# Optimization experiments

Measured on AMD Instinct MI355X. Metric: run time of the kernel, lower is better.

The kernel has to match this reference:

```python
import jax, jax.numpy as jnp
import numpy as np

# tcnn Hash-grid config from TropicalHashGrid.__init__ defaults
L = 16          # n_levels
F = 2           # n_features_per_level
T = 19          # log2_hashmap_size
N_MIN = 16      # base_resolution
N_MAX = 2048
SCALE = 1.0
HASHMAP = 1 << T
B = 2.0 ** (np.log2(N_MAX * SCALE / N_MIN) / (L - 1))  # per-level scale
PRIMES = np.array([1, 2654435761, 805459861], dtype=np.uint32)
# 8 trilinear corner offsets in {0,1}^3
CORNERS = np.stack(np.meshgrid(*([np.arange(2)] * 3), indexing='ij'), axis=-1).reshape(8, 3)
N_POINTS = 2 ** 21


def _level_encode(x, tbl, scale, res, dense):
    """One hash-grid level: x [N,3], tbl [HASHMAP,F] -> [N,F]."""
    pos = x * scale + 0.5                      # tcnn convention
    pf = jnp.floor(pos)
    frac = pos - pf                            # [N,3]
    grid = pf.astype(jnp.int32)                # [N,3]
    idx = grid[:, None, :] + jnp.asarray(CORNERS, jnp.int32)[None]  # [N,8,3]
    if dense:
        # coarse level fits densely: stride indexing x + y*res + z*res^2
        idx = jnp.minimum(idx, res - 1)
        flat = idx[..., 0] + idx[..., 1] * res + idx[..., 2] * (res * res)
    else:
        # spatial hash: xor of coordinate * prime, masked to table size
        u = idx.astype(jnp.uint32)
        flat = ((u[..., 0] * PRIMES[0]) ^ (u[..., 1] * PRIMES[1]) ^ (u[..., 2] * PRIMES[2]))
        flat = (flat & jnp.uint32(HASHMAP - 1)).astype(jnp.int32)
    feats = tbl[flat]                          # [N,8,F] gather
    c = jnp.asarray(CORNERS, jnp.float32)
    w = jnp.prod(jnp.where(c[None] > 0, frac[:, None, :], 1.0 - frac[:, None, :]), axis=-1)  # [N,8]
    return jnp.einsum('nc,ncf->nf', w, feats)  # trilinear blend


def setup_inputs() -> dict:
    key = jax.random.key(0)
    k1, k2 = jax.random.split(key)
    x = jax.random.uniform(k1, (N_POINTS, 3), dtype=jnp.float32)  # coords in [0,1)^3
    # hash table params (tcnn inits ~U(-1e-4,1e-4); scaled randn equivalent scale)
    table = jax.random.normal(k2, (L, HASHMAP, F), dtype=jnp.float32) * 1e-4
    return {"x": x, "table": table}


def reference(x, table):
    outs = []
    for l in range(L):
        scale = float(N_MIN * (B ** l) - 1.0)   # grid_scale per tcnn/_marks
        res = int(np.ceil(scale)) + 1
        dense = (res ** 3) <= HASHMAP
        outs.append(_level_encode(x, table[l], scale, res, dense))
    return jnp.concatenate(outs, axis=-1)        # [N, L*F]
```

## Files before the change

### kernel.cpp

```cpp
#include <hip/hip_runtime.h>
#include <cstdint>
#include <cmath>


typedef float    f32x2 __attribute__((ext_vector_type(2)));
typedef float    f32x4 __attribute__((ext_vector_type(4)));
typedef uint32_t u32x2 __attribute__((ext_vector_type(2)));
typedef uint32_t u32x4 __attribute__((ext_vector_type(4)));
typedef _Float16 h16x2 __attribute__((ext_vector_type(2)));

#define NLEVELS 16
#define HASHMAP (1 << 19)
#define HMASK ((uint32_t)(HASHMAP - 1))
#define PRIME_Y 2654435761u
#define PRIME_Z 805459861u
#define F16SCALE 1024.0f
#define F16UNSCALE (1.0f / 1024.0f)

struct HGParams {
    float scale[NLEVELS];
    int   res[NLEVELS];
    int   dense[NLEVELS];
    int   dpk_off[NLEVELS];
    int   hq_off[NLEVELS];
    int   dq_off[NLEVELS];
};

__device__ __forceinline__ uint32_t sel4(u32x4 q, uint32_t k) {
    const uint32_t a = (k & 1u) ? q.y : q.x;
    const uint32_t b = (k & 1u) ? q.w : q.z;
    return (k & 2u) ? b : a;
}
__device__ __forceinline__ void unpack_h2(uint32_t w, float& lo, float& hi) {
    const h16x2 h = __builtin_bit_cast(h16x2, w);
    lo = (float)h.x; hi = (float)h.y;
}
__device__ __forceinline__ uint32_t pack_h2(float a, float b) {
    h16x2 h; h.x = (_Float16)a; h.y = (_Float16)b;
    return __builtin_bit_cast(uint32_t, h);
}

__global__ __launch_bounds__(256) void repack_hashed_f16(
    const f32x4* __restrict__ table2, uint32_t* __restrict__ hqw, HGParams p)
{
    const int l = blockIdx.y;
    if (p.hq_off[l] < 0) return;
    const f32x4* __restrict__ src = table2 + (size_t)l * (HASHMAP / 2);
    u32x2* __restrict__ dst = (u32x2*)(hqw + (size_t)p.hq_off[l] * 4);
    for (int k = blockIdx.x * 256 + threadIdx.x; k < HASHMAP / 2;
         k += gridDim.x * 256) {
        const f32x4 v = src[k];
        u32x2 w;
        w.x = pack_h2(v.x * F16SCALE, v.y * F16SCALE);
        w.y = pack_h2(v.z * F16SCALE, v.w * F16SCALE);
        dst[k] = w;
    }
}

__global__ __launch_bounds__(256) void repack_dense_f16(
    const f32x2* __restrict__ table, u32x4* __restrict__ dqt, HGParams p)
{
    const int l = blockIdx.y;
    if (p.dq_off[l] < 0) return;
    const int res = p.res[l];
    const int rm = res - 1;
    const int r2 = res * res;
    const int res3 = r2 * res;
    const f32x2* __restrict__ src = table + (size_t)l * HASHMAP;
    u32x4* __restrict__ dst = dqt + p.dq_off[l];
    for (int k = blockIdx.x * 256 + threadIdx.x; k < res3;
         k += gridDim.x * 256) {
        const int x = k % res;
        const int t = k / res;
        const int y = t % res;
        const int dx = (x < rm) ? 1 : 0;
        const int dy = (y < rm) ? res : 0;
        const f32x2 e00 = src[k];
        const f32x2 e10 = src[k + dx];
        const f32x2 e01 = src[k + dy];
        const f32x2 e11 = src[k + dx + dy];
        u32x4 w;
        w.x = pack_h2(e00.x * F16SCALE, e00.y * F16SCALE);
        w.y = pack_h2(e10.x * F16SCALE, e10.y * F16SCALE);
        w.z = pack_h2(e01.x * F16SCALE, e01.y * F16SCALE);
        w.w = pack_h2(e11.x * F16SCALE, e11.y * F16SCALE);
        dst[k] = w;
    }
}

__global__ __launch_bounds__(256) void repack_dense_k(
    const f32x2* __restrict__ table, f32x4* __restrict__ dpk, HGParams p)
{
    const int l = blockIdx.y;
    if (!p.dense[l] || p.dpk_off[l] < 0) return;
    const int res = p.res[l];
    const int res3 = res * res * res;
    const f32x2* __restrict__ src = table + (size_t)l * HASHMAP;
    f32x4* __restrict__ dst = dpk + p.dpk_off[l];
    for (int k = blockIdx.x * 256 + threadIdx.x; k < res3; k += gridDim.x * 256) {
        const f32x2 a = src[k];
        const f32x2 b = src[k + 1];
        f32x4 v; v.x = a.x; v.y = a.y; v.z = b.x; v.w = b.y;
        dst[k] = v;
    }
}

__device__ __forceinline__ void point_fp32(
    const f32x2* __restrict__ tbl, const f32x4* __restrict__ dpkt,
    bool dense, int res,
    float rx, float ry, float rz, int ix, int iy, int iz,
    float& ox, float& oy)
{
    const float wx0 = 1.0f - rx, wx1 = rx;
    const float wy_[2] = {1.0f - ry, ry};
    const float wz_[2] = {1.0f - rz, rz};
    float ax = 0.0f, ay = 0.0f;
    if (dense) {
        const int rm = res - 1;
        const int x0 = min(ix, rm), x1 = min(ix + 1, rm);
        const int y0 = min(iy, rm), y1 = min(iy + 1, rm);
        const int z0 = min(iz, rm), z1 = min(iz + 1, rm);
        const int r2 = res * res;
        const int ys[2] = {y0 * res, y1 * res};
        const int zs[2] = {z0 * r2,  z1 * r2};
        const int d = x1 - x0;
        if (dpkt) {
            f32x4 f4[4];
#pragma unroll
            for (int c = 0; c < 4; ++c)
                f4[c] = dpkt[x0 + ys[(c >> 1) & 1] + zs[c & 1]];
#pragma unroll
            for (int c = 0; c < 4; ++c) {
                const f32x2 c0 = f4[c].xy;
                const f32x2 c1 = d ? f4[c].zw : f4[c].xy;
                const float wyz = wy_[(c >> 1) & 1] * wz_[c & 1];
                ax += wyz * (wx0 * c0.x + wx1 * c1.x);
                ay += wyz * (wx0 * c0.y + wx1 * c1.y);
            }
        } else {
            f32x2 f0[4], f1[4];
#pragma unroll
            for (int c = 0; c < 4; ++c) {
                const int b = ys[(c >> 1) & 1] + zs[c & 1];
                f0[c] = tbl[x0 + b];
                f1[c] = tbl[x1 + b];
            }
#pragma unroll
            for (int c = 0; c < 4; ++c) {
                const float wyz = wy_[(c >> 1) & 1] * wz_[c & 1];
                ax += wyz * (wx0 * f0[c].x + wx1 * f1[c].x);
                ay += wyz * (wx0 * f0[c].y + wx1 * f1[c].y);
            }
        }
    } else {
        const uint32_t ux = (uint32_t)ix;
        const uint32_t hy[2] = {(uint32_t)iy * PRIME_Y, (uint32_t)(iy + 1) * PRIME_Y};
        const uint32_t hz[2] = {(uint32_t)iz * PRIME_Z, (uint32_t)(iz + 1) * PRIME_Z};
        uint32_t H0[4], H1[4];
#pragma unroll
        for (int c = 0; c < 4; ++c) {
            const uint32_t hyz = hy[(c >> 1) & 1] ^ hz[c & 1];
            H0[c] = (ux ^ hyz) & HMASK;
            H1[c] = ((ux + 1u) ^ hyz) & HMASK;
        }
        const f32x4* __restrict__ t4 = (const f32x4*)tbl;
        f32x4 f4[4];
#pragma unroll
        for (int c = 0; c < 4; ++c) f4[c] = t4[H0[c] >> 1];
        f32x2 c1v[4];
        if (ux & 1u) {
#pragma unroll
            for (int c = 0; c < 4; ++c) c1v[c] = tbl[H1[c]];
        } else {
#pragma unroll
            for (int c = 0; c < 4; ++c)
                c1v[c] = (H0[c] & 1u) ? f4[c].xy : f4[c].zw;
        }
#pragma unroll
        for (int c = 0; c < 4; ++c) {
            const f32x2 c0 = (H0[c] & 1u) ? f4[c].zw : f4[c].xy;
            const float wyz = wy_[(c >> 1) & 1] * wz_[c & 1];
            ax += wyz * (wx0 * c0.x + wx1 * c1v[c].x);
            ay += wyz * (wx0 * c0.y + wx1 * c1v[c].y);
        }
    }
    ox = ax; oy = ay;
}

__global__ __launch_bounds__(256, 6) void hashgrid_level(
    const float* __restrict__ x,
    const float* __restrict__ table,
    const f32x4* __restrict__ dpk,
    const u32x4* __restrict__ hq,
    const u32x4* __restrict__ dq,
    f32x2* __restrict__ dst,
    HGParams p,
    int npoints,
    size_t stride_l,
    size_t stride_n)
{
    __shared__ float sx[1536];
    const int tid = threadIdx.x;
    const int base = blockIdx.x << 9;
    const int l = blockIdx.y;

    const int total = npoints * 3;
    const int sbase = base * 3;
#pragma unroll
    for (int k = 0; k < 6; ++k) {
        const int li = tid + (k << 8);
        const int gi = sbase + li;
        sx[li] = (gi < total) ? x[gi] : 0.0f;
    }
    __syncthreads();

    const int n0 = base + (tid << 1);
    if (n0 >= npoints) return;
    const bool pair = (n0 + 1) < npoints;

    const float scale = p.scale[l];
    const int   res   = p.res[l];
    const bool  dense = (p.dense[l] != 0);

    float rx[2], ry[2], rz[2];
    int ixv[2], iyv[2], izv[2];
#pragma unroll
    for (int j = 0; j < 2; ++j) {
        const int s = ((tid << 1) | j) * 3;
        const float px = sx[s + 0] * scale + 0.5f;
        const float py = sx[s + 1] * scale + 0.5f;
        const float pz = sx[s + 2] * scale + 0.5f;
        const float fx = floorf(px), fy = floorf(py), fz = floorf(pz);
        rx[j] = px - fx; ry[j] = py - fy; rz[j] = pz - fz;
        ixv[j] = (int)fx; iyv[j] = (int)fy; izv[j] = (int)fz;
    }

    float ox[2], oy[2];

    if (dense && dq && p.dq_off[l] >= 0) {
        const u32x4* __restrict__ dt = dq + p.dq_off[l];
        const int rm = res - 1, r2 = res * res;
        u32x4 qa[2], qb[2];
#pragma unroll
        for (int j = 0; j < 2; ++j) {
            const int x0 = min(ixv[j], rm), y0 = min(iyv[j], rm);
            const int z0 = min(izv[j], rm), z1 = min(izv[j] + 1, rm);
            const int b = x0 + y0 * res;
            qa[j] = dt[b + z0 * r2];
            qb[j] = dt[b + z1 * r2];
        }
#pragma unroll
        for (int j = 0; j < 2; ++j) {
            const float wx0 = 1.0f - rx[j], wx1 = rx[j];
            const float wy0 = 1.0f - ry[j], wy1 = ry[j];
            const float wz0 = 1.0f - rz[j], wz1 = rz[j];
            float a00x, a00y, a10x, a10y, a01x, a01y, a11x, a11y;
            unpack_h2(qa[j].x, a00x, a00y);
            unpack_h2(qa[j].y, a10x, a10y);
            unpack_h2(qa[j].z, a01x, a01y);
            unpack_h2(qa[j].w, a11x, a11y);
            const float bax = wy0 * (wx0 * a00x + wx1 * a10x)
                            + wy1 * (wx0 * a01x + wx1 * a11x);
            const float bay = wy0 * (wx0 * a00y + wx1 * a10y)
                            + wy1 * (wx0 * a01y + wx1 * a11y);
            float b00x, b00y, b10x, b10y, b01x, b01y, b11x, b11y;
            unpack_h2(qb[j].x, b00x, b00y);
            unpack_h2(qb[j].y, b10x, b10y);
            unpack_h2(qb[j].z, b01x, b01y);
            unpack_h2(qb[j].w, b11x, b11y);
            const float bbx = wy0 * (wx0 * b00x + wx1 * b10x)
                            + wy1 * (wx0 * b01x + wx1 * b11x);
            const float bby = wy0 * (wx0 * b00y + wx1 * b10y)
                            + wy1 * (wx0 * b01y + wx1 * b11y);
            ox[j] = (wz0 * bax + wz1 * bbx) * F16UNSCALE;
            oy[j] = (wz0 * bay + wz1 * bby) * F16UNSCALE;
        }
    } else if (!dense && hq && p.hq_off[l] >= 0) {
        const u32x4* __restrict__ ht = hq + p.hq_off[l];
        const uint32_t* __restrict__ htw = (const uint32_t*)ht;
        uint32_t H0[2][4], dxm[2];
#pragma unroll
        for (int j = 0; j < 2; ++j) {
            const uint32_t ux = (uint32_t)ixv[j];
            const uint32_t hy0 = (uint32_t)iyv[j] * PRIME_Y;
            const uint32_t hy1 = (uint32_t)(iyv[j] + 1) * PRIME_Y;
            const uint32_t hz0 = (uint32_t)izv[j] * PRIME_Z;
            const uint32_t hz1 = (uint32_t)(izv[j] + 1) * PRIME_Z;
#pragma unroll
            for (int c = 0; c < 4; ++c) {
                const uint32_t hyz = ((c & 2) ? hy1 : hy0) ^ ((c & 1) ? hz1 : hz0);
                H0[j][c] = (ux ^ hyz) & HMASK;
            }
            dxm[j] = (ux ^ (ux + 1u)) & HMASK;
        }
        u32x4 q0[2][4];
#pragma unroll
        for (int j = 0; j < 2; ++j)
#pragma unroll
            for (int c = 0; c < 4; ++c)
                q0[j][c] = ht[H0[j][c] >> 2];
        uint32_t sE[2][4];
#pragma unroll
        for (int j = 0; j < 2; ++j) {
            if (dxm[j] >= 4u) {
#pragma unroll
                for (int c = 0; c < 4; ++c)
                    sE[j][c] = htw[H0[j][c] ^ dxm[j]];
            }
        }
#pragma unroll
        for (int j = 0; j < 2; ++j) {
            const float wx0 = 1.0f - rx[j], wx1 = rx[j];
            const float wy0 = 1.0f - ry[j], wy1 = ry[j];
            const float wz0 = 1.0f - rz[j], wz1 = rz[j];
            const bool st = (dxm[j] >= 4u);
            float ax = 0.0f, ay = 0.0f;
#pragma unroll
            for (int c = 0; c < 4; ++c) {
                const uint32_t k0 = H0[j][c] & 3u;
                const uint32_t e0 = sel4(q0[j][c], k0);
                const uint32_t e1 = st ? sE[j][c]
                                       : sel4(q0[j][c], k0 ^ (dxm[j] & 3u));
                float c0x, c0y, c1x, c1y;
                unpack_h2(e0, c0x, c0y);
                unpack_h2(e1, c1x, c1y);
                const float wyz = ((c & 2) ? wy1 : wy0) * ((c & 1) ? wz1 : wz0);
                ax += wyz * (wx0 * c0x + wx1 * c1x);
                ay += wyz * (wx0 * c0y + wx1 * c1y);
            }
            ox[j] = ax * F16UNSCALE;
            oy[j] = ay * F16UNSCALE;
        }
    } else {
        const f32x2* __restrict__ tbl =
            (const f32x2*)table + (size_t)l * (size_t)HASHMAP;
        const f32x4* __restrict__ dpkt =
            (dense && dpk && p.dpk_off[l] >= 0) ? (dpk + p.dpk_off[l]) : nullptr;
#pragma unroll
        for (int j = 0; j < 2; ++j)
            point_fp32(tbl, dpkt, dense, res,
                       rx[j], ry[j], rz[j], ixv[j], iyv[j], izv[j],
                       ox[j], oy[j]);
    }

    const size_t db = (size_t)l * stride_l;
    if (pair && stride_n == 1) {
        f32x4 v; v.x = ox[0]; v.y = oy[0]; v.z = ox[1]; v.w = oy[1];
        __builtin_nontemporal_store(v, (f32x4*)(dst + db + (size_t)n0));
    } else {
        f32x2 a; a.x = ox[0]; a.y = oy[0];
        __builtin_nontemporal_store(a, dst + db + (size_t)n0 * stride_n);
        if (pair) {
            f32x2 b2; b2.x = ox[1]; b2.y = oy[1];
            __builtin_nontemporal_store(b2, dst + db + (size_t)(n0 + 1) * stride_n);
        }
    }
}

__global__ __launch_bounds__(256) void transpose_out(
    const f32x4* __restrict__ ws4,
    f32x4* __restrict__ out4,
    int npoints)
{
    __shared__ f32x2 tile[NLEVELS][130];
    const int tid = threadIdx.x;
    const int base = blockIdx.x << 7;
    const int np2 = npoints >> 1;

#pragma unroll
    for (int k = 0; k < 4; ++k) {
        const int flat = tid + (k << 8);
        const int l  = flat >> 6;
        const int pr = flat & 63;
        const int gp = (base >> 1) + pr;
        if (gp < np2) {
            const f32x4 v = __builtin_nontemporal_load(ws4 + (size_t)l * np2 + gp);
            tile[l][2 * pr]     = v.xy;
            tile[l][2 * pr + 1] = v.zw;
        }
    }
    __syncthreads();

#pragma unroll
    for (int k = 0; k < 4; ++k) {
        const int flat = tid + (k << 8);
        const int nl = flat >> 3;
        const int c  = flat & 7;
        const int nn = base + nl;
        if (nn < npoints) {
            const f32x2 a = tile[2 * c][nl];
            const f32x2 b = tile[2 * c + 1][nl];
            f32x4 v; v.x = a.x; v.y = a.y; v.z = b.x; v.w = b.y;
            __builtin_nontemporal_store(v, out4 + (size_t)nn * 8 + c);
        }
    }
}

extern "C" void kernel_launch(void* const* d_in, const int* in_sizes, int n_in,
                              void* d_out, int out_size, void* d_ws, size_t ws_size,
                              hipStream_t stream) {
    const float* x     = (const float*)d_in[0];
    const float* table = (const float*)d_in[1];
    float* out         = (float*)d_out;
    const int npoints  = in_sizes[0] / 3;

    HGParams p;
    const double B = pow(2.0, 7.0 / 15.0);
    int dpk_total = 0;
    int dq_total = 0;
    int hq_total = 0;
    int max_res3 = 0;
    for (int l = 0; l < NLEVELS; ++l) {
        const double s = 16.0 * pow(B, (double)l) - 1.0;
        p.scale[l] = (float)s;
        const int res = (int)ceil(s) + 1;
        p.res[l] = res;
        const long long r3 = (long long)res * res * res;
        p.dense[l] = (r3 <= (long long)HASHMAP) ? 1 : 0;
        if (p.dense[l]) {
            p.dpk_off[l] = dpk_total;  dpk_total += (int)r3;
            p.dq_off[l]  = dq_total;   dq_total  += (int)r3;
            p.hq_off[l]  = -1;
            if ((int)r3 > max_res3) max_res3 = (int)r3;
        } else {
            p.dpk_off[l] = -1;
            p.dq_off[l]  = -1;
            p.hq_off[l]  = hq_total;   hq_total  += HASHMAP / 4;
        }
    }

    const size_t need_main = (size_t)npoints * NLEVELS * sizeof(f32x2);
    const bool ws_main = (ws_size >= need_main) && ((npoints & 1) == 0);
    const size_t off0 = ws_main ? need_main : 0;

    const size_t hq_bytes = (size_t)hq_total * 16;
    const size_t dq_bytes = (size_t)dq_total * 16;
    const bool tierA = (ws_size >= off0 + hq_bytes + dq_bytes);

    const u32x4* hq = nullptr;
    const u32x4* dq = nullptr;
    const f32x4* dpk = nullptr;

    if (tierA) {
        uint32_t* hqw = (uint32_t*)((char*)d_ws + off0);
        u32x4*    dqt = (u32x4*)((char*)d_ws + off0 + hq_bytes);
        hq = (const u32x4*)hqw;
        dq = dqt;
        {
            const dim3 gr(1024, NLEVELS);
            repack_hashed_f16<<<gr, 256, 0, stream>>>(
                (const f32x4*)table, hqw, p);
        }
        {
            const dim3 gr((max_res3 + 255) / 256, NLEVELS);
            repack_dense_f16<<<gr, 256, 0, stream>>>(
                (const f32x2*)table, dqt, p);
        }
    } else {
        for (int l = 0; l < NLEVELS; ++l) { p.hq_off[l] = -1; p.dq_off[l] = -1; }
        const size_t need_dpk = (size_t)dpk_total * sizeof(f32x4);
        const bool use_dpk = (ws_size >= off0 + need_dpk) && dpk_total > 0;
        if (use_dpk) {
            f32x4* dpkw = (f32x4*)((char*)d_ws + off0);
            dpk = dpkw;
            const dim3 gr((max_res3 + 255) / 256, NLEVELS);
            repack_dense_k<<<gr, 256, 0, stream>>>((const f32x2*)table, dpkw, p);
        } else {
            for (int l = 0; l < NLEVELS; ++l) p.dpk_off[l] = -1;
        }
    }

    const dim3 g1((npoints + 511) / 512, NLEVELS);
    if (ws_main) {
        hashgrid_level<<<g1, 256, 0, stream>>>(
            x, table, dpk, hq, dq, (f32x2*)d_ws, p, npoints,
            (size_t)npoints, (size_t)1);
        const int nb2 = (npoints + 127) / 128;
        transpose_out<<<nb2, 256, 0, stream>>>(
            (const f32x4*)d_ws, (f32x4*)out, npoints);
    } else {
        hashgrid_level<<<g1, 256, 0, stream>>>(
            x, table, dpk, hq, dq, (f32x2*)out, p, npoints,
            (size_t)1, (size_t)NLEVELS);
    }
}
```

Baseline: 933.0 us.

## Store intermediate level outputs as fp16 and fuse repack kernels

The per-level intermediate buffer is now stored as packed fp16 (scaled by 1024) instead of fp32, which halves the write and read traffic between the level kernel and the transpose kernel. The transpose kernel is rewritten to unpack fp16 and handle 256 points per block. The two repack kernels are merged into one launch, and the occupancy hint of 6 is dropped from the level kernel's launch bounds. Storing outputs in fp16 adds quantization error to the final result.

```diff
diff --git a/kernel.cpp b/kernel.cpp
--- a/kernel.cpp
+++ b/kernel.cpp
@@ -40,51 +40,51 @@
     return __builtin_bit_cast(uint32_t, h);
 }
 
-__global__ __launch_bounds__(256) void repack_hashed_f16(
-    const f32x4* __restrict__ table2, uint32_t* __restrict__ hqw, HGParams p)
+__global__ __launch_bounds__(256) void repack_all_f16(
+    const float* __restrict__ table, uint32_t* __restrict__ hqw,
+    u32x4* __restrict__ dqt, HGParams p)
 {
     const int l = blockIdx.y;
-    if (p.hq_off[l] < 0) return;
-    const f32x4* __restrict__ src = table2 + (size_t)l * (HASHMAP / 2);
-    u32x2* __restrict__ dst = (u32x2*)(hqw + (size_t)p.hq_off[l] * 4);
-    for (int k = blockIdx.x * 256 + threadIdx.x; k < HASHMAP / 2;
-         k += gridDim.x * 256) {
-        const f32x4 v = src[k];
-        u32x2 w;
-        w.x = pack_h2(v.x * F16SCALE, v.y * F16SCALE);
-        w.y = pack_h2(v.z * F16SCALE, v.w * F16SCALE);
-        dst[k] = w;
-    }
-}
-
-__global__ __launch_bounds__(256) void repack_dense_f16(
-    const f32x2* __restrict__ table, u32x4* __restrict__ dqt, HGParams p)
-{
-    const int l = blockIdx.y;
-    if (p.dq_off[l] < 0) return;
-    const int res = p.res[l];
-    const int rm = res - 1;
-    const int r2 = res * res;
-    const int res3 = r2 * res;
-    const f32x2* __restrict__ src = table + (size_t)l * HASHMAP;
-    u32x4* __restrict__ dst = dqt + p.dq_off[l];
-    for (int k = blockIdx.x * 256 + threadIdx.x; k < res3;
-         k += gridDim.x * 256) {
-        const int x = k % res;
-        const int t = k / res;
-        const int y = t % res;
-        const int dx = (x < rm) ? 1 : 0;
-        const int dy = (y < rm) ? res : 0;
-        const f32x2 e00 = src[k];
-        const f32x2 e10 = src[k + dx];
-        const f32x2 e01 = src[k + dy];
-        const f32x2 e11 = src[k + dx + dy];
-        u32x4 w;
-        w.x = pack_h2(e00.x * F16SCALE, e00.y * F16SCALE);
-        w.y = pack_h2(e10.x * F16SCALE, e10.y * F16SCALE);
-        w.z = pack_h2(e01.x * F16SCALE, e01.y * F16SCALE);
-        w.w = pack_h2(e11.x * F16SCALE, e11.y * F16SCALE);
-        dst[k] = w;
+    if (p.dense[l]) {
+        if (p.dq_off[l] < 0) return;
+        const int res = p.res[l];
+        const int rm = res - 1;
+        const int r2 = res * res;
+        const int res3 = r2 * res;
+        const f32x2* __restrict__ src =
+            (const f32x2*)table + (size_t)l * HASHMAP;
+        u32x4* __restrict__ dst = dqt + p.dq_off[l];
+        for (int k = blockIdx.x * 256 + threadIdx.x; k < res3;
+             k += gridDim.x * 256) {
+            const int x = k % res;
+            const int t = k / res;
+            const int y = t % res;
+            const int dx = (x < rm) ? 1 : 0;
+            const int dy = (y < rm) ? res : 0;
+            const f32x2 e00 = src[k];
+            const f32x2 e10 = src[k + dx];
+            const f32x2 e01 = src[k + dy];
+            const f32x2 e11 = src[k + dx + dy];
+            u32x4 w;
+            w.x = pack_h2(e00.x * F16SCALE, e00.y * F16SCALE);
+            w.y = pack_h2(e10.x * F16SCALE, e10.y * F16SCALE);
+            w.z = pack_h2(e01.x * F16SCALE, e01.y * F16SCALE);
+            w.w = pack_h2(e11.x * F16SCALE, e11.y * F16SCALE);
+            dst[k] = w;
+        }
+    } else {
+        if (p.hq_off[l] < 0) return;
+        const f32x4* __restrict__ src =
+            (const f32x4*)table + (size_t)l * (HASHMAP / 2);
+        u32x2* __restrict__ dst = (u32x2*)(hqw + (size_t)p.hq_off[l] * 4);
+        for (int k = blockIdx.x * 256 + threadIdx.x; k < HASHMAP / 2;
+             k += gridDim.x * 256) {
+            const f32x4 v = src[k];
+            u32x2 w;
+            w.x = pack_h2(v.x * F16SCALE, v.y * F16SCALE);
+            w.y = pack_h2(v.z * F16SCALE, v.w * F16SCALE);
+            dst[k] = w;
+        }
     }
 }
 
@@ -184,20 +184,19 @@
             ay += wyz * (wx0 * c0.y + wx1 * c1v[c].y);
         }
     }
-    ox = ax; oy = ay;
-}
-
-__global__ __launch_bounds__(256, 6) void hashgrid_level(
+    ox = ax * F16SCALE; oy = ay * F16SCALE;
+}
+
+__global__ __launch_bounds__(256) void hashgrid_level(
     const float* __restrict__ x,
     const float* __restrict__ table,
     const f32x4* __restrict__ dpk,
     const u32x4* __restrict__ hq,
     const u32x4* __restrict__ dq,
-    f32x2* __restrict__ dst,
+    f32x2* __restrict__ dst32,
+    uint32_t* __restrict__ dsth,
     HGParams p,
-    int npoints,
-    size_t stride_l,
-    size_t stride_n)
+    int npoints)
 {
     __shared__ float sx[1536];
     const int tid = threadIdx.x;
@@ -272,8 +271,8 @@
                             + wy1 * (wx0 * b01x + wx1 * b11x);
             const float bby = wy0 * (wx0 * b00y + wx1 * b10y)
                             + wy1 * (wx0 * b01y + wx1 * b11y);
-            ox[j] = (wz0 * bax + wz1 * bbx) * F16UNSCALE;
-            oy[j] = (wz0 * bay + wz1 * bby) * F16UNSCALE;
+            ox[j] = wz0 * bax + wz1 * bbx;
+            oy[j] = wz0 * bay + wz1 * bby;
         }
     } else if (!dense && hq && p.hq_off[l] >= 0) {
         const u32x4* __restrict__ ht = hq + p.hq_off[l];
@@ -328,8 +327,8 @@
                 ax += wyz * (wx0 * c0x + wx1 * c1x);
                 ay += wyz * (wx0 * c0y + wx1 * c1y);
             }
-            ox[j] = ax * F16UNSCALE;
-            oy[j] = ay * F16UNSCALE;
+            ox[j] = ax;
+            oy[j] = ay;
         }
     } else {
         const f32x2* __restrict__ tbl =
@@ -343,54 +342,61 @@
                        ox[j], oy[j]);
     }
 
-    const size_t db = (size_t)l * stride_l;
-    if (pair && stride_n == 1) {
-        f32x4 v; v.x = ox[0]; v.y = oy[0]; v.z = ox[1]; v.w = oy[1];
-        __builtin_nontemporal_store(v, (f32x4*)(dst + db + (size_t)n0));
-    } else {
-        f32x2 a; a.x = ox[0]; a.y = oy[0];
-        __builtin_nontemporal_store(a, dst + db + (size_t)n0 * stride_n);
+    if (dsth) {
+        u32x2 w;
+        w.x = pack_h2(ox[0], oy[0]);
+        w.y = pack_h2(ox[1], oy[1]);
+        __builtin_nontemporal_store(
+            w, (u32x2*)(dsth + (size_t)l * npoints + n0));
+    } else {
+        f32x2 a; a.x = ox[0] * F16UNSCALE; a.y = oy[0] * F16UNSCALE;
+        __builtin_nontemporal_store(a, dst32 + (size_t)n0 * NLEVELS + l);
         if (pair) {
-            f32x2 b2; b2.x = ox[1]; b2.y = oy[1];
-            __builtin_nontemporal_store(b2, dst + db + (size_t)(n0 + 1) * stride_n);
-        }
-    }
-}
-
-__global__ __launch_bounds__(256) void transpose_out(
-    const f32x4* __restrict__ ws4,
+            f32x2 b2; b2.x = ox[1] * F16UNSCALE; b2.y = oy[1] * F16UNSCALE;
+            __builtin_nontemporal_store(b2, dst32 + (size_t)(n0 + 1) * NLEVELS + l);
+        }
+    }
+}
+
+__global__ __launch_bounds__(256) void transpose_out_f16(
+    const u32x4* __restrict__ ws4,
     f32x4* __restrict__ out4,
     int npoints)
 {
-    __shared__ f32x2 tile[NLEVELS][130];
+    __shared__ uint32_t tile[NLEVELS][260];
     const int tid = threadIdx.x;
-    const int base = blockIdx.x << 7;
-    const int np2 = npoints >> 1;
+    const int base = blockIdx.x << 8;
+    const int np4 = npoints >> 2;
 
 #pragma unroll
     for (int k = 0; k < 4; ++k) {
-        const int flat = tid + (k << 8);
-        const int l  = flat >> 6;
-        const int pr = flat & 63;
-        const int gp = (base >> 1) + pr;
-        if (gp < np2) {
-            const f32x4 v = __builtin_nontemporal_load(ws4 + (size_t)l * np2 + gp);
-            tile[l][2 * pr]     = v.xy;
-            tile[l][2 * pr + 1] = v.zw;
+        const int f = tid + (k << 8);
+        const int lv = f >> 6;
+        const int p4 = f & 63;
+        const int gp = (base >> 2) + p4;
+        if (gp < np4) {
+            const u32x4 v = __builtin_nontemporal_load(ws4 + (size_t)lv * np4 + gp);
+            tile[lv][4 * p4 + 0] = v.x;
+            tile[lv][4 * p4 + 1] = v.y;
+            tile[lv][4 * p4 + 2] = v.z;
+            tile[lv][4 * p4 + 3] = v.w;
         }
     }
     __syncthreads();
 
 #pragma unroll
-    for (int k = 0; k < 4; ++k) {
-        const int flat = tid + (k << 8);
-        const int nl = flat >> 3;
-        const int c  = flat & 7;
-        const int nn = base + nl;
+    for (int k = 0; k < 8; ++k) {
+        const int f = tid + (k << 8);
+        const int pl = f >> 3;
+        const int c  = f & 7;
+        const int nn = base + pl;
         if (nn < npoints) {
-            const f32x2 a = tile[2 * c][nl];
-            const f32x2 b = tile[2 * c + 1][nl];
-            f32x4 v; v.x = a.x; v.y = a.y; v.z = b.x; v.w = b.y;
+            float ax, ay, bx, by;
+            unpack_h2(tile[2 * c][pl],     ax, ay);
+            unpack_h2(tile[2 * c + 1][pl], bx, by);
+            f32x4 v;
+            v.x = ax * F16UNSCALE; v.y = ay * F16UNSCALE;
+            v.z = bx * F16UNSCALE; v.w = by * F16UNSCALE;
             __builtin_nontemporal_store(v, out4 + (size_t)nn * 8 + c);
         }
     }
@@ -429,8 +435,8 @@
         }
     }
 
-    const size_t need_main = (size_t)npoints * NLEVELS * sizeof(f32x2);
-    const bool ws_main = (ws_size >= need_main) && ((npoints & 1) == 0);
+    const size_t need_main = (size_t)npoints * NLEVELS * sizeof(uint32_t);
+    const bool ws_main = (ws_size >= need_main) && ((npoints & 3) == 0);
     const size_t off0 = ws_main ? need_main : 0;
 
     const size_t hq_bytes = (size_t)hq_total * 16;
@@ -446,16 +452,11 @@
         u32x4*    dqt = (u32x4*)((char*)d_ws + off0 + hq_bytes);
         hq = (const u32x4*)hqw;
         dq = dqt;
-        {
-            const dim3 gr(1024, NLEVELS);
-            repack_hashed_f16<<<gr, 256, 0, stream>>>(
-                (const f32x4*)table, hqw, p);
-        }
-        {
-            const dim3 gr((max_res3 + 255) / 256, NLEVELS);
-            repack_dense_f16<<<gr, 256, 0, stream>>>(
-                (const f32x2*)table, dqt, p);
-        }
+        const int gx_h = (HASHMAP / 2 + 255) / 256;
+        const int gx_d = (max_res3 + 255) / 256;
+        const int gx = gx_h > gx_d ? gx_h : gx_d;
+        const dim3 gr(gx, NLEVELS);
+        repack_all_f16<<<gr, 256, 0, stream>>>(table, hqw, dqt, p);
     } else {
         for (int l = 0; l < NLEVELS; ++l) { p.hq_off[l] = -1; p.dq_off[l] = -1; }
         const size_t need_dpk = (size_t)dpk_total * sizeof(f32x4);
@@ -473,14 +474,12 @@
     const dim3 g1((npoints + 511) / 512, NLEVELS);
     if (ws_main) {
         hashgrid_level<<<g1, 256, 0, stream>>>(
-            x, table, dpk, hq, dq, (f32x2*)d_ws, p, npoints,
-            (size_t)npoints, (size_t)1);
-        const int nb2 = (npoints + 127) / 128;
-        transpose_out<<<nb2, 256, 0, stream>>>(
-            (const f32x4*)d_ws, (f32x4*)out, npoints);
+            x, table, dpk, hq, dq, nullptr, (uint32_t*)d_ws, p, npoints);
+        const int nb2 = (npoints + 255) / 256;
+        transpose_out_f16<<<nb2, 256, 0, stream>>>(
+            (const u32x4*)d_ws, (f32x4*)out, npoints);
     } else {
         hashgrid_level<<<g1, 256, 0, stream>>>(
-            x, table, dpk, hq, dq, (f32x2*)out, p, npoints,
-            (size_t)1, (size_t)NLEVELS);
-    }
-}
+            x, table, dpk, hq, dq, (f32x2*)out, nullptr, p, npoints);
+    }
+}
```

After: 916.5 us. About the same (-1.8%).
